# Kernel tuning notes

Hardware: AMD Instinct MI355X
Metric: run time of the kernel (lower is better)

Reference implementation:

```python
import jax, jax.numpy as jnp
from jax import lax
import numpy as np

B, L, C_IN, HID, RANK, NC = 256, 1024, 16, 512, 128, 10
PAD, K = 4, 7  # each conv block: L -> L + 2*PAD - K + 1 = L + 2


def _block(x, dwk, dwb, pwk, pwb, g, b):
    # x: (B, C, L); depthwise conv (groups=C) -> pointwise 1x1 -> batchnorm (batch stats) -> relu
    cin = dwk.shape[0]
    dn = ('NCH', 'OIH', 'NCH')
    y = lax.conv_general_dilated(x, dwk, (1,), [(PAD, PAD)], dimension_numbers=dn,
                                 feature_group_count=cin) + dwb[None, :, None]
    y = lax.conv_general_dilated(y, pwk, (1,), [(0, 0)], dimension_numbers=dn) + pwb[None, :, None]
    m = y.mean(axis=(0, 2), keepdims=True)
    v = y.var(axis=(0, 2), keepdims=True)
    y = (y - m) * lax.rsqrt(v + 1e-5) * g[None, :, None] + b[None, :, None]
    return jax.nn.relu(y)


def _cell(xp, h, c, Ui, Vi, Uh, Vh, bi, bh):
    # low-rank LSTM cell: W = U @ V kept factored for efficiency (same math)
    gates = (xp @ Ui) @ Vi + bi + (h @ Uh) @ Vh + bh  # (B, 4H)
    i, f, g, o = jnp.split(gates, 4, axis=1)
    c = jax.nn.sigmoid(f) * c + jax.nn.sigmoid(i) * jnp.tanh(g)
    h = jax.nn.sigmoid(o) * jnp.tanh(c)
    return h, c


def _forward(x, dw_k1, dw_b1, pw_k1, pw_b1, bn_g1, bn_b1,
             dw_k2, dw_b2, pw_k2, pw_b2, bn_g2, bn_b2,
             dw_k3, dw_b3, pw_k3, pw_b3, bn_g3, bn_b3,
             dw_k4, dw_b4, pw_k4, pw_b4, bn_g4, bn_b4,
             Ui1, Vi1, Uh1, Vh1, bi1, bh1,
             Ui2, Vi2, Uh2, Vh2, bi2, bh2,
             fc_w, fc_b):
    y = x[:, 0].transpose(0, 2, 1)  # (B, C_IN, L)
    y = _block(y, dw_k1, dw_b1, pw_k1, pw_b1, bn_g1, bn_b1)
    y = _block(y, dw_k2, dw_b2, pw_k2, pw_b2, bn_g2, bn_b2)
    y = _block(y, dw_k3, dw_b3, pw_k3, pw_b3, bn_g3, bn_b3)
    y = _block(y, dw_k4, dw_b4, pw_k4, pw_b4, bn_g4, bn_b4)
    # dropout = identity (eval)
    xs = y.transpose(2, 0, 1)  # (T, B, 32), T = L + 8
    bsz = xs.shape[1]
    z = jnp.zeros((bsz, HID), xs.dtype)

    def step(carry, xt):
        h1, c1, h2, c2 = carry
        h1, c1 = _cell(xt, h1, c1, Ui1, Vi1, Uh1, Vh1, bi1, bh1)
        h2, c2 = _cell(h1, h2, c2, Ui2, Vi2, Uh2, Vh2, bi2, bh2)
        return (h1, c1, h2, c2), None

    (h1, c1, h2, c2), _ = lax.scan(step, (z, z, z, z), xs)
    # original stacks all h2 then takes [:, -1, :] -> final h2; dropout = identity
    return h2 @ fc_w.T + fc_b  # (B, NC)


def setup_inputs() -> dict:
    key = jax.random.key(0)
    ks = iter(jax.random.split(key, 64))

    def n(shape, scale=0.05):
        return jax.random.normal(next(ks), shape, jnp.float32) * scale

    inp = {'x': jax.random.normal(next(ks), (B, 1, L, C_IN), jnp.float32)}
    chans = [C_IN, 32, 32, 32]
    for i, cin in enumerate(chans, start=1):
        inp[f'dw_k{i}'] = n((cin, 1, K))
        inp[f'dw_b{i}'] = jnp.zeros((cin,), jnp.float32)
        inp[f'pw_k{i}'] = n((32, cin, 1))
        inp[f'pw_b{i}'] = jnp.zeros((32,), jnp.float32)
        inp[f'bn_g{i}'] = jnp.ones((32,), jnp.float32)
        inp[f'bn_b{i}'] = jnp.zeros((32,), jnp.float32)
    inp['Ui1'] = n((32, RANK)); inp['Vi1'] = n((RANK, 4 * HID))
    inp['Uh1'] = n((HID, RANK)); inp['Vh1'] = n((RANK, 4 * HID))
    inp['bi1'] = jnp.zeros((4 * HID,), jnp.float32); inp['bh1'] = jnp.zeros((4 * HID,), jnp.float32)
    inp['Ui2'] = n((HID, RANK)); inp['Vi2'] = n((RANK, 4 * HID))
    inp['Uh2'] = n((HID, RANK)); inp['Vh2'] = n((RANK, 4 * HID))
    inp['bi2'] = jnp.zeros((4 * HID,), jnp.float32); inp['bh2'] = jnp.zeros((4 * HID,), jnp.float32)
    inp['fc_w'] = n((NC, HID)); inp['fc_b'] = jnp.zeros((NC,), jnp.float32)
    return inp


def reference(x, dw_k1, dw_b1, pw_k1, pw_b1, bn_g1, bn_b1,
              dw_k2, dw_b2, pw_k2, pw_b2, bn_g2, bn_b2,
              dw_k3, dw_b3, pw_k3, pw_b3, bn_g3, bn_b3,
              dw_k4, dw_b4, pw_k4, pw_b4, bn_g4, bn_b4,
              Ui1, Vi1, Uh1, Vh1, bi1, bh1,
              Ui2, Vi2, Uh2, Vh2, bi2, bh2,
              fc_w, fc_b):
    return _forward(x, dw_k1, dw_b1, pw_k1, pw_b1, bn_g1, bn_b1,
                    dw_k2, dw_b2, pw_k2, pw_b2, bn_g2, bn_b2,
                    dw_k3, dw_b3, pw_k3, pw_b3, bn_g3, bn_b3,
                    dw_k4, dw_b4, pw_k4, pw_b4, bn_g4, bn_b4,
                    Ui1, Vi1, Uh1, Vh1, bi1, bh1,
                    Ui2, Vi2, Uh2, Vh2, bi2, bh2,
                    fc_w, fc_b)
```

## Files before the change

### kernel.cpp

```cpp
#include <hip/hip_runtime.h>
#include <stdint.h>
#include <stddef.h>
#include <limits.h>

typedef _Float16 f16;
typedef _Float16 half8 __attribute__((ext_vector_type(8)));
typedef float floatx4 __attribute__((ext_vector_type(4)));
typedef unsigned long long u64;

#define MFMA(a,b,c) __builtin_amdgcn_mfma_f32_16x16x32_f16((a),(b),(c),0,0,0)

static constexpr int LMAX   = 1032;
static constexpr int TSTEPS = 1032;

static constexpr size_t ZBYTES   = (size_t)256*32*LMAX*2;
static constexpr size_t OFF_ZA   = 0;
static constexpr size_t OFF_ZB   = OFF_ZA + ZBYTES;
static constexpr size_t OFF_Y4   = OFF_ZA;
static constexpr size_t OFF_WH1F = OFF_ZB + ZBYTES;
static constexpr size_t OFF_WI2F = OFF_WH1F + (size_t)128*16*64*8*2;
static constexpr size_t OFF_WH2F = OFF_WI2F + (size_t)128*16*64*8*2;
static constexpr size_t OFF_WX1F = OFF_WH2F + (size_t)128*16*64*8*2;
static constexpr size_t OFF_B1   = OFF_WX1F + (size_t)128*64*8*2;
static constexpr size_t OFF_B2   = OFF_B1 + (size_t)2048*4;
static constexpr size_t OFF_STATS= OFF_B2 + (size_t)2048*4;
static constexpr size_t OFF_AB   = OFF_STATS + (size_t)4*64*4;
static constexpr size_t OFF_H1X  = OFF_AB + (size_t)4*64*4;
static constexpr size_t OFF_H2X  = OFF_H1X + (size_t)8*8*32*512*2;
static constexpr size_t OFF_FLAGS= OFF_H2X + (size_t)8*4*32*512*2;

__device__ __forceinline__ float sigm(float x){ return 1.f/(1.f+__expf(-x)); }
__device__ __forceinline__ float tanh_f(float x){ float e=__expf(2.f*x); return (e-1.f)/(e+1.f); }

__device__ __forceinline__ void sta64(void* p, u64 v){
  __hip_atomic_store((u64*)p, v, __ATOMIC_RELAXED, __HIP_MEMORY_SCOPE_AGENT);
}
__device__ __forceinline__ u64 lda64(const void* p){
  return __hip_atomic_load((const u64*)p, __ATOMIC_RELAXED, __HIP_MEMORY_SCOPE_AGENT);
}
__device__ __forceinline__ uint32_t ldf(const uint32_t* p){
  return __hip_atomic_load(p, __ATOMIC_RELAXED, __HIP_MEMORY_SCOPE_AGENT);
}
__device__ __forceinline__ void stf(uint32_t* p, uint32_t v){
  __hip_atomic_store(p, v, __ATOMIC_RELAXED, __HIP_MEMORY_SCOPE_AGENT);
}
__device__ __forceinline__ float4 ldg16(const void* p){
  float4 r;
  asm volatile("global_load_dwordx4 %0, %1, off sc0 sc1" : "=v"(r) : "v"(p) : "memory");
  return r;
}
__device__ __forceinline__ void vmcnt0(){
  asm volatile("s_waitcnt vmcnt(0)" ::: "memory");
}

__device__ __forceinline__ void pollWave(const uint32_t* fl, int t1, int t2){
  const int lane = threadIdx.x & 63;
  int tgt = (lane < 16) ? t1 : ((lane < 32) ? t2 : INT_MIN);
  if (tgt <= 0) tgt = INT_MIN;
  while (true){
    uint32_t v = ldf(&fl[lane & 31]);
    if (__all((int)v >= tgt)) break;
    __builtin_amdgcn_s_sleep(1);
  }
}

__device__ __forceinline__ void stageIssue(float4* r, const f16* src, int tid){
  #pragma unroll
  for (int i=0;i<8;++i){
    int qq = tid + 256*i;
    r[i] = ldg16(src + (size_t)qq*8);
  }
}
__device__ __forceinline__ void stageWrite(uint8_t* base, const float4* r, int tid){
  #pragma unroll
  for (int i=0;i<8;++i){
    int qq = tid + 256*i;
    int row = qq >> 6, ck = qq & 63;
    int cs = ck ^ (row & 15);
    *(float4*)(base + ((row<<6) + cs)*16) = r[i];
  }
}
__device__ __forceinline__ half8 fragLDS(const uint8_t* base, int row, int q, int lq){
  return *(const half8*)(base + (((row<<6)) + (((q<<2)+lq) ^ (row & 15)))*16);
}

__global__ void k_zero(float* stats, uint32_t* flags){
  int bx = blockIdx.x, tid = threadIdx.x;
  if (bx == 4){ if (tid < 256) stats[tid] = 0.f; }
  else flags[bx*256 + tid] = 0u;
}

__global__ __launch_bounds__(256) void k_prep_W(f16* __restrict__ dst, const float* __restrict__ U, const float* __restrict__ V){
  __shared__ float sU[64][65];
  __shared__ float sV[64][68];
  const int tid = threadIdx.x;
  const int n0 = blockIdx.x*64, k0 = blockIdx.y*64;
  const int tx = tid & 15, ty = tid >> 4;
  float acc[4][4];
  #pragma unroll
  for (int a=0;a<4;++a){ acc[a][0]=0.f; acc[a][1]=0.f; acc[a][2]=0.f; acc[a][3]=0.f; }
  for (int rc=0; rc<2; ++rc){
    __syncthreads();
    #pragma unroll
    for (int i=0;i<16;++i){
      int f = tid + 256*i;
      int row = f>>6, col = f&63;
      sU[row][col] = U[(size_t)(k0+row)*128 + rc*64 + col];
      sV[row][col] = V[(size_t)(rc*64+row)*2048 + n0 + col];
    }
    __syncthreads();
    for (int rr=0; rr<64; ++rr){
      float4 bv = *(const float4*)&sV[rr][tx*4];
      #pragma unroll
      for (int a=0;a<4;++a){
        float av = sU[ty*4+a][rr];
        acc[a][0] += av*bv.x; acc[a][1] += av*bv.y; acc[a][2] += av*bv.z; acc[a][3] += av*bv.w;
      }
    }
  }
  #pragma unroll
  for (int a=0;a<4;++a){
    int k = k0 + ty*4 + a;
    int q = k>>5, lq2 = (k>>3)&3, j = k&7;
    #pragma unroll
    for (int c=0;c<4;++c){
      int n = n0 + tx*4 + c;
      int nt = n>>4, lmn = n&15;
      dst[(((size_t)nt*16 + q)*64 + (lq2*16+lmn))*8 + j] = (f16)acc[a][c];
    }
  }
}

__global__ __launch_bounds__(256) void k_prep_Wx(f16* __restrict__ dst, const float* __restrict__ U, const float* __restrict__ V){
  __shared__ float sU[32][129];
  __shared__ float sV[128][68];
  const int tid = threadIdx.x, n0 = blockIdx.x*64;
  for (int f=tid; f<32*128; f+=256) sU[f>>7][f&127] = U[f];
  for (int f=tid; f<128*64; f+=256) sV[f>>6][f&63] = V[(size_t)(f>>6)*2048 + n0 + (f&63)];
  __syncthreads();
  int nn = tid & 63, kb = (tid>>6)*8;
  int n = n0 + nn;
  float acc[8];
  #pragma unroll
  for (int i=0;i<8;++i) acc[i]=0.f;
  for (int r=0;r<128;++r){
    float v = sV[r][nn];
    #pragma unroll
    for (int i=0;i<8;++i) acc[i] += sU[kb+i][r]*v;
  }
  int nt = n>>4, lmn = n&15;
  #pragma unroll
  for (int i=0;i<8;++i){
    int k = kb+i;
    dst[((size_t)nt*64 + (((k>>3)&3)*16 + lmn))*8 + (k&7)] = (f16)acc[i];
  }
}

__global__ void k_prep_bias(float* dst, const float* a, const float* b){
  int idx = blockIdx.x*256 + threadIdx.x;
  if (idx < 2048) dst[idx] = a[idx] + b[idx];
}

__global__ __launch_bounds__(256) void k_conv(
    const float* __restrict__ x0, const f16* __restrict__ zin,
    const float* __restrict__ abp,
    const float* __restrict__ dwk, const float* __restrict__ dwb,
    const float* __restrict__ pwk, const float* __restrict__ pwb,
    f16* __restrict__ zout, float* __restrict__ stats,
    int Lin, int Cin)
{
  const int tid = threadIdx.x;
  const int b = blockIdx.y;
  const int l = blockIdx.x*256 + tid;
  const int Lout = Lin + 2;
  __shared__ float sPw[32*32], sDw[32*7], sDb[32], sPb[32], sAb[64];
  __shared__ float sRed[2][4][32];
  for (int i=tid; i<Cin*32; i+=256) sPw[i] = pwk[i];
  for (int i=tid; i<Cin*7;  i+=256) sDw[i] = dwk[i];
  if (tid < Cin) sDb[tid] = dwb[tid];
  if (tid >= 64 && tid < 96) sPb[tid-64] = pwb[tid-64];
  if (abp != nullptr && tid >= 128 && tid < 192) sAb[tid-128] = abp[tid-128];
  __syncthreads();

  float acc[32];
  #pragma unroll
  for (int o=0;o<32;++o) acc[o] = sPb[o];
  const bool act = (l < Lout);
  if (act){
    for (int c=0;c<Cin;++c){
      float s = sDb[c];
      #pragma unroll
      for (int k=0;k<7;++k){
        int li = l + k - 4;
        float v = 0.f;
        if (li >= 0 && li < Lin){
          if (x0) v = x0[((size_t)b*1024 + li)*16 + c];
          else {
            float z = (float)zin[((size_t)b*32 + c)*LMAX + li];
            v = fmaxf(sAb[c]*z + sAb[32+c], 0.f);
          }
        }
        s += sDw[c*7+k]*v;
      }
      #pragma unroll
      for (int o=0;o<32;++o) acc[o] += sPw[o*Cin + c]*s;
    }
    #pragma unroll
    for (int o=0;o<32;++o) zout[((size_t)b*32 + o)*LMAX + l] = (f16)acc[o];
  }
  const int lane = tid & 63, wv = tid >> 6;
  for (int o=0;o<32;++o){
    float v = act ? acc[o] : 0.f;
    float q = v*v;
    #pragma unroll
    for (int m=1;m<64;m<<=1){ v += __shfl_xor(v,m); q += __shfl_xor(q,m); }
    if (lane == 0){ sRed[0][wv][o] = v; sRed[1][wv][o] = q; }
  }
  __syncthreads();
  if (tid < 32){
    float v = sRed[0][0][tid]+sRed[0][1][tid]+sRed[0][2][tid]+sRed[0][3][tid];
    float q = sRed[1][0][tid]+sRed[1][1][tid]+sRed[1][2][tid]+sRed[1][3][tid];
    atomicAdd(&stats[tid], v);
    atomicAdd(&stats[32+tid], q);
  }
}

__global__ void k_bnfin(const float* __restrict__ stats, const float* __restrict__ g,
                        const float* __restrict__ beta, float* __restrict__ ab, float inv_n)
{
  int o = threadIdx.x;
  if (o < 32){
    float m = stats[o]*inv_n;
    float var = stats[32+o]*inv_n - m*m;
    float a = g[o]*rsqrtf(var + 1e-5f);
    ab[o] = a; ab[32+o] = beta[o] - m*a;
  }
}

__global__ __launch_bounds__(256) void k_y4(const f16* __restrict__ z, const float* __restrict__ ab, f16* __restrict__ y){
  __shared__ f16 sT[32][264];
  __shared__ float sA[64];
  const int b = blockIdx.x, t0 = blockIdx.y*256, tid = threadIdx.x;
  if (tid < 64) sA[tid] = ab[tid];
  __syncthreads();
  #pragma unroll
  for (int i=0;i<8;++i){
    int f = tid + 256*i;
    int ch = f >> 6, tq = f & 63;
    int t = t0 + tq*4;
    if (t < 1032){
      u64 v = *(const u64*)(z + ((size_t)(b*32+ch)*1032 + t));
      union { u64 u; f16 h[4]; } cv; cv.u = v;
      float a = sA[ch], bb = sA[32+ch];
      #pragma unroll
      for (int j=0;j<4;++j) cv.h[j] = (f16)fmaxf(a*(float)cv.h[j] + bb, 0.f);
      *(u64*)&sT[ch][tq*4] = cv.u;
    }
  }
  __syncthreads();
  int t = t0 + tid;
  if (t < 1032){
    union { uint4 v; f16 h[8]; } o[4];
    #pragma unroll
    for (int k=0;k<4;++k)
      #pragma unroll
      for (int j=0;j<8;++j) o[k].h[j] = sT[k*8+j][t - t0];
    uint4* dst = (uint4*)(y + ((size_t)b*1032 + t)*32);
    #pragma unroll
    for (int k=0;k<4;++k) dst[k] = o[k].v;
  }
}

__global__ __launch_bounds__(256,1) void k_lstm(
  const f16* __restrict__ y4x,
  const f16* __restrict__ Wx1F, const f16* __restrict__ Wh1F,
  const f16* __restrict__ Wi2F, const f16* __restrict__ Wh2F,
  const float* __restrict__ bias1, const float* __restrict__ bias2,
  f16* __restrict__ h1x, f16* __restrict__ h2x,
  uint32_t* __restrict__ flags,
  const float* __restrict__ fcw, const float* __restrict__ fcb,
  float* __restrict__ outp)
{
  const int tid  = threadIdx.x;
  const int lane = tid & 63;
  const int w    = tid >> 6;
  const int lm   = lane & 15;
  const int lq   = lane >> 4;
  const int lq8  = lq*8;
  const int g    = blockIdx.x & 7;
  const int idx  = blockIdx.x >> 3;
  const int role = idx >> 4;
  const int b    = idx & 15;

  __shared__ __align__(16) uint8_t bufA[32768];
  __shared__ __align__(16) uint8_t bufB[32768];
  __shared__ float sGate[4*32*33];

  uint32_t* fl = flags + (size_t)g*32;

  const float* biasL = role ? bias2 : bias1;
  float bs[2];
  #pragma unroll
  for (int ct=0; ct<2; ++ct) bs[ct] = biasL[w*512 + b*32 + ct*16 + lm];

  const int nt0 = w*32 + b*2;
  f16* hdst_base = role ? h2x + (size_t)g*4*32*512 : h1x + (size_t)g*8*32*512;

  float creg[4] = {0.f,0.f,0.f,0.f};
  const int cr_row = tid >> 3, cr_u0 = (tid & 7)*4;

  if (role == 0){
    half8 wx[2];
    half8 wB[2][16];
    #pragma unroll
    for (int ct=0; ct<2; ++ct){
      wx[ct] = *(const half8*)&Wx1F[((size_t)(nt0+ct)*64 + lane)*8];
      #pragma unroll
      for (int q=0;q<16;++q)
        wB[ct][q] = *(const half8*)&Wh1F[(((size_t)(nt0+ct)*16 + q)*64 + lane)*8];
    }
    #pragma unroll 1
    for (int t=0; t<TSTEPS; ++t){
      half8 ya0 = *(const half8*)(y4x + ((size_t)(g*32 + lm)*1032 + t)*32 + lq8);
      half8 ya1 = *(const half8*)(y4x + ((size_t)(g*32 + 16 + lm)*1032 + t)*32 + lq8);
      if (w == 0) pollWave(fl, t, t-7);
      __syncthreads();
      float4 st[8];
      if (t >= 1) stageIssue(st, h1x + ((size_t)(g*8 + ((t-1)&7))*32*512), tid);
      floatx4 acc[2][2];
      #pragma unroll
      for (int ct=0; ct<2; ++ct){
        acc[ct][0] = (floatx4){bs[ct],bs[ct],bs[ct],bs[ct]};
        acc[ct][1] = acc[ct][0];
      }
      acc[0][0] = MFMA(ya0, wx[0], acc[0][0]);
      acc[0][1] = MFMA(ya1, wx[0], acc[0][1]);
      acc[1][0] = MFMA(ya0, wx[1], acc[1][0]);
      acc[1][1] = MFMA(ya1, wx[1], acc[1][1]);
      if (t >= 1){
        vmcnt0();
        stageWrite(bufA, st, tid);
      }
      __syncthreads();
      if (t >= 1){
        #pragma unroll
        for (int q=0;q<16;++q){
          half8 a0 = fragLDS(bufA, lm,    q, lq);
          half8 a1 = fragLDS(bufA, 16+lm, q, lq);
          acc[0][0] = MFMA(a0, wB[0][q], acc[0][0]);
          acc[0][1] = MFMA(a1, wB[0][q], acc[0][1]);
          acc[1][0] = MFMA(a0, wB[1][q], acc[1][0]);
          acc[1][1] = MFMA(a1, wB[1][q], acc[1][1]);
        }
      }
      __syncthreads();
      #pragma unroll
      for (int ct=0; ct<2; ++ct)
        #pragma unroll
        for (int rt=0; rt<2; ++rt)
          #pragma unroll
          for (int r=0;r<4;++r)
            sGate[w*1056 + (rt*16 + lq*4 + r)*33 + ct*16 + lm] = acc[ct][rt][r];
      __syncthreads();
      {
        union { u64 uu; f16 h[4]; } hv;
        #pragma unroll
        for (int j=0;j<4;++j){
          int u = cr_u0 + j;
          float iv = sGate[0*1056 + cr_row*33 + u];
          float fv = sGate[1*1056 + cr_row*33 + u];
          float gv = sGate[2*1056 + cr_row*33 + u];
          float ov = sGate[3*1056 + cr_row*33 + u];
          float c = sigm(fv)*creg[j] + sigm(iv)*tanh_f(gv);
          creg[j] = c;
          hv.h[j] = (f16)(sigm(ov)*tanh_f(c));
        }
        f16* dst = hdst_base + (size_t)(t&7)*32*512 + cr_row*512 + b*32 + cr_u0;
        sta64(dst, hv.uu);
      }
      vmcnt0();
      __syncthreads();
      if (tid == 0) stf(&fl[b], (uint32_t)(t+1));
    }
  } else {
    half8 wA[2][16];
    half8 wB[2][16];
    #pragma unroll
    for (int ct=0; ct<2; ++ct)
      #pragma unroll
      for (int q=0;q<16;++q){
        wA[ct][q] = *(const half8*)&Wi2F[(((size_t)(nt0+ct)*16 + q)*64 + lane)*8];
        wB[ct][q] = *(const half8*)&Wh2F[(((size_t)(nt0+ct)*16 + q)*64 + lane)*8];
      }
    #pragma unroll 1
    for (int t=0; t<TSTEPS; ++t){
      if (w == 0) pollWave(fl, t+1, t);
      __syncthreads();
      float4 s0[8], s1[8];
      stageIssue(s0, h1x + ((size_t)(g*8 + (t&7))*32*512), tid);
      if (t >= 1) stageIssue(s1, h2x + ((size_t)(g*4 + ((t-1)&3))*32*512), tid);
      vmcnt0();
      stageWrite(bufA, s0, tid);
      if (t >= 1) stageWrite(bufB, s1, tid);
      __syncthreads();
      floatx4 acc[2][2];
      #pragma unroll
      for (int ct=0; ct<2; ++ct){
        acc[ct][0] = (floatx4){bs[ct],bs[ct],bs[ct],bs[ct]};
        acc[ct][1] = acc[ct][0];
      }
      #pragma unroll
      for (int q=0;q<16;++q){
        half8 a0 = fragLDS(bufA, lm,    q, lq);
        half8 a1 = fragLDS(bufA, 16+lm, q, lq);
        acc[0][0] = MFMA(a0, wA[0][q], acc[0][0]);
        acc[0][1] = MFMA(a1, wA[0][q], acc[0][1]);
        acc[1][0] = MFMA(a0, wA[1][q], acc[1][0]);
        acc[1][1] = MFMA(a1, wA[1][q], acc[1][1]);
      }
      if (t >= 1){
        #pragma unroll
        for (int q=0;q<16;++q){
          half8 a0 = fragLDS(bufB, lm,    q, lq);
          half8 a1 = fragLDS(bufB, 16+lm, q, lq);
          acc[0][0] = MFMA(a0, wB[0][q], acc[0][0]);
          acc[0][1] = MFMA(a1, wB[0][q], acc[0][1]);
          acc[1][0] = MFMA(a0, wB[1][q], acc[1][0]);
          acc[1][1] = MFMA(a1, wB[1][q], acc[1][1]);
        }
      }
      __syncthreads();
      #pragma unroll
      for (int ct=0; ct<2; ++ct)
        #pragma unroll
        for (int rt=0; rt<2; ++rt)
          #pragma unroll
          for (int r=0;r<4;++r)
            sGate[w*1056 + (rt*16 + lq*4 + r)*33 + ct*16 + lm] = acc[ct][rt][r];
      __syncthreads();
      {
        union { u64 uu; f16 h[4]; } hv;
        #pragma unroll
        for (int j=0;j<4;++j){
          int u = cr_u0 + j;
          float iv = sGate[0*1056 + cr_row*33 + u];
          float fv = sGate[1*1056 + cr_row*33 + u];
          float gv = sGate[2*1056 + cr_row*33 + u];
          float ov = sGate[3*1056 + cr_row*33 + u];
          float c = sigm(fv)*creg[j] + sigm(iv)*tanh_f(gv);
          creg[j] = c;
          hv.h[j] = (f16)(sigm(ov)*tanh_f(c));
        }
        f16* dst = hdst_base + (size_t)(t&3)*32*512 + cr_row*512 + b*32 + cr_u0;
        sta64(dst, hv.uu);
      }
      vmcnt0();
      __syncthreads();
      if (tid == 0) stf(&fl[16 + b], (uint32_t)(t+1));
    }
    if (b == 0){
      if (w == 0) pollWave(fl, 0, TSTEPS);
      __syncthreads();
      const f16* hbase = h2x + ((size_t)(g*4 + ((TSTEPS-1)&3))*32*512);
      for (int e = tid; e < 320; e += 256){
        int row = e/10, nc = e%10;
        float s = fcb[nc];
        const float* wv = fcw + (size_t)nc*512;
        const u64* hp = (const u64*)(hbase + row*512);
        for (int k4=0;k4<128;++k4){
          union { u64 uu; f16 h[4]; } cv; cv.uu = lda64(hp + k4);
          #pragma unroll
          for (int i2=0;i2<4;++i2) s += (float)cv.h[i2]*wv[k4*4+i2];
        }
        outp[(size_t)(g*32+row)*10 + nc] = s;
      }
    }
  }
}

extern "C" void kernel_launch(void* const* d_in, const int* in_sizes, int n_in,
                              void* d_out, int out_size, void* d_ws, size_t ws_size,
                              hipStream_t stream)
{
  (void)in_sizes; (void)n_in; (void)out_size; (void)ws_size;
  const float* x = (const float*)d_in[0];
  auto F = [&](int i){ return (const float*)d_in[i]; };
  const float *Ui1=F(25), *Vi1=F(26), *Uh1=F(27), *Vh1=F(28), *bi1=F(29), *bh1=F(30);
  const float *Ui2=F(31), *Vi2=F(32), *Uh2=F(33), *Vh2=F(34), *bi2=F(35), *bh2=F(36);
  const float *fcw=F(37), *fcb=F(38);

  uint8_t* ws = (uint8_t*)d_ws;
  f16* zA   = (f16*)(ws + OFF_ZA);
  f16* zB   = (f16*)(ws + OFF_ZB);
  f16* y4x  = (f16*)(ws + OFF_Y4);
  f16* Wh1F = (f16*)(ws + OFF_WH1F);
  f16* Wi2F = (f16*)(ws + OFF_WI2F);
  f16* Wh2F = (f16*)(ws + OFF_WH2F);
  f16* Wx1F = (f16*)(ws + OFF_WX1F);
  float* bias1 = (float*)(ws + OFF_B1);
  float* bias2 = (float*)(ws + OFF_B2);
  float* stats = (float*)(ws + OFF_STATS);
  float* ab    = (float*)(ws + OFF_AB);
  f16* h1x  = (f16*)(ws + OFF_H1X);
  f16* h2x  = (f16*)(ws + OFF_H2X);
  uint32_t* flags = (uint32_t*)(ws + OFF_FLAGS);
  float* outp = (float*)d_out;

  k_zero<<<5, 256, 0, stream>>>(stats, flags);

  k_prep_W<<<dim3(32,8), 256, 0, stream>>>(Wh1F, Uh1, Vh1);
  k_prep_W<<<dim3(32,8), 256, 0, stream>>>(Wi2F, Ui2, Vi2);
  k_prep_W<<<dim3(32,8), 256, 0, stream>>>(Wh2F, Uh2, Vh2);
  k_prep_Wx<<<32, 256, 0, stream>>>(Wx1F, Ui1, Vi1);
  k_prep_bias<<<8, 256, 0, stream>>>(bias1, bi1, bh1);
  k_prep_bias<<<8, 256, 0, stream>>>(bias2, bi2, bh2);

  dim3 cgrid(5, 256);
  k_conv<<<cgrid, 256, 0, stream>>>(x, nullptr, nullptr, F(1), F(2), F(3), F(4),
                                    zA, stats + 0*64, 1024, 16);
  k_bnfin<<<1, 64, 0, stream>>>(stats + 0*64, F(5), F(6), ab + 0*64, 1.f/(256.f*1026.f));
  k_conv<<<cgrid, 256, 0, stream>>>(nullptr, zA, ab + 0*64, F(7), F(8), F(9), F(10),
                                    zB, stats + 1*64, 1026, 32);
  k_bnfin<<<1, 64, 0, stream>>>(stats + 1*64, F(11), F(12), ab + 1*64, 1.f/(256.f*1028.f));
  k_conv<<<cgrid, 256, 0, stream>>>(nullptr, zB, ab + 1*64, F(13), F(14), F(15), F(16),
                                    zA, stats + 2*64, 1028, 32);
  k_bnfin<<<1, 64, 0, stream>>>(stats + 2*64, F(17), F(18), ab + 2*64, 1.f/(256.f*1030.f));
  k_conv<<<cgrid, 256, 0, stream>>>(nullptr, zA, ab + 2*64, F(19), F(20), F(21), F(22),
                                    zB, stats + 3*64, 1030, 32);
  k_bnfin<<<1, 64, 0, stream>>>(stats + 3*64, F(23), F(24), ab + 3*64, 1.f/(256.f*1032.f));

  k_y4<<<dim3(256,5), 256, 0, stream>>>(zB, ab + 3*64, y4x);

  k_lstm<<<256, 256, 0, stream>>>(y4x,
                                  Wx1F, Wh1F, Wi2F, Wh2F,
                                  bias1, bias2,
                                  h1x, h2x, flags,
                                  fcw, fcb, outp);
}
```

Measured before the change: 6.149 ms.

## Keep LSTM weights low-rank and exchange rank projections via fixed-point atomic rings

The recurrent kernel no longer multiplies by dense 512x2048 weights rebuilt from U@V. Each block projects its hidden slice onto the rank-128 factor U and reduces partial projections across blocks with 64-bit fixed-point atomicAdd into zeroed ring buffers, then applies V locally. The batch split changes from 8 groups of 32 to 16 groups of 16 with 512-thread blocks, and gate math runs directly in MFMA registers instead of through shared memory. This cuts per-step matmul work and the volume of hidden state exchanged between blocks. In exchange it adds atomic traffic, ring zeroing, a fixed-point rounding error, and a deeper dependency chain per timestep.

Result: slower. 8.462 ms (+37.6%).

```diff
diff --git a/kernel.cpp b/kernel.cpp
--- a/kernel.cpp
+++ b/kernel.cpp
@@ -7,30 +7,45 @@
 typedef _Float16 half8 __attribute__((ext_vector_type(8)));
 typedef float floatx4 __attribute__((ext_vector_type(4)));
 typedef unsigned long long u64;
+typedef unsigned int u32;
 
 #define MFMA(a,b,c) __builtin_amdgcn_mfma_f32_16x16x32_f16((a),(b),(c),0,0,0)
 
 static constexpr int LMAX   = 1032;
 static constexpr int TSTEPS = 1032;
+
+static constexpr float FXSCALE = 1048576.0f;
+static constexpr float FXINV   = 1.0f/1048576.0f;
+static constexpr int   FXBIAS  = 1<<28;
+static constexpr int   FXBIAS4 = 1<<30;
 
 static constexpr size_t ZBYTES   = (size_t)256*32*LMAX*2;
 static constexpr size_t OFF_ZA   = 0;
 static constexpr size_t OFF_ZB   = OFF_ZA + ZBYTES;
 static constexpr size_t OFF_Y4   = OFF_ZA;
-static constexpr size_t OFF_WH1F = OFF_ZB + ZBYTES;
-static constexpr size_t OFF_WI2F = OFF_WH1F + (size_t)128*16*64*8*2;
-static constexpr size_t OFF_WH2F = OFF_WI2F + (size_t)128*16*64*8*2;
-static constexpr size_t OFF_WX1F = OFF_WH2F + (size_t)128*16*64*8*2;
-static constexpr size_t OFF_B1   = OFF_WX1F + (size_t)128*64*8*2;
-static constexpr size_t OFF_B2   = OFF_B1 + (size_t)2048*4;
-static constexpr size_t OFF_STATS= OFF_B2 + (size_t)2048*4;
-static constexpr size_t OFF_AB   = OFF_STATS + (size_t)4*64*4;
-static constexpr size_t OFF_H1X  = OFF_AB + (size_t)4*64*4;
-static constexpr size_t OFF_H2X  = OFF_H1X + (size_t)8*8*32*512*2;
-static constexpr size_t OFF_FLAGS= OFF_H2X + (size_t)8*4*32*512*2;
+static constexpr size_t OFF_WXF  = OFF_ZB + ZBYTES;
+static constexpr size_t OFF_VH1F = OFF_WXF  + 131072;
+static constexpr size_t OFF_VI2F = OFF_VH1F + 524288;
+static constexpr size_t OFF_VH2F = OFF_VI2F + 524288;
+static constexpr size_t OFF_UH1F = OFF_VH2F + 524288;
+static constexpr size_t OFF_UI2F = OFF_UH1F + 131072;
+static constexpr size_t OFF_UH2F = OFF_UI2F + 131072;
+static constexpr size_t OFF_B1   = OFF_UH2F + 131072;
+static constexpr size_t OFF_B2   = OFF_B1 + 8192;
+static constexpr size_t OFF_STATS= OFF_B2 + 8192;
+static constexpr size_t OFF_AB   = OFF_STATS + 1024;
+static constexpr size_t OFF_RINGS= OFF_AB + 1024;
+static constexpr size_t RING_BYTES = (size_t)16*24576*8;
+static constexpr size_t OFF_H2F  = OFF_RINGS + RING_BYTES;
+static constexpr size_t OFF_FLAGS= OFF_H2F + 262144;
 
 __device__ __forceinline__ float sigm(float x){ return 1.f/(1.f+__expf(-x)); }
-__device__ __forceinline__ float tanh_f(float x){ float e=__expf(2.f*x); return (e-1.f)/(e+1.f); }
+__device__ __forceinline__ float tanh_f(float x){
+  float ax = fabsf(x);
+  float e = __expf(-2.f*ax);
+  float r = (1.f - e)/(1.f + e);
+  return (x < 0.f) ? -r : r;
+}
 
 __device__ __forceinline__ void sta64(void* p, u64 v){
   __hip_atomic_store((u64*)p, v, __ATOMIC_RELAXED, __HIP_MEMORY_SCOPE_AGENT);
@@ -44,116 +59,96 @@
 __device__ __forceinline__ void stf(uint32_t* p, uint32_t v){
   __hip_atomic_store(p, v, __ATOMIC_RELAXED, __HIP_MEMORY_SCOPE_AGENT);
 }
-__device__ __forceinline__ float4 ldg16(const void* p){
-  float4 r;
+__device__ __forceinline__ int4 ldg16i(const void* p){
+  int4 r;
   asm volatile("global_load_dwordx4 %0, %1, off sc0 sc1" : "=v"(r) : "v"(p) : "memory");
   return r;
 }
 __device__ __forceinline__ void vmcnt0(){
   asm volatile("s_waitcnt vmcnt(0)" ::: "memory");
 }
-
-__device__ __forceinline__ void pollWave(const uint32_t* fl, int t1, int t2){
+__device__ __forceinline__ void schedbar(){
+  __builtin_amdgcn_sched_barrier(0);
+}
+
+__device__ __forceinline__ void pollWave8(const uint32_t* fl, int tP, int tC){
   const int lane = threadIdx.x & 63;
-  int tgt = (lane < 16) ? t1 : ((lane < 32) ? t2 : INT_MIN);
+  int tgt = (lane < 4) ? tP : ((lane < 8) ? tC : INT_MIN);
   if (tgt <= 0) tgt = INT_MIN;
   while (true){
-    uint32_t v = ldf(&fl[lane & 31]);
+    uint32_t v = ldf(&fl[lane & 7]);
     if (__all((int)v >= tgt)) break;
     __builtin_amdgcn_s_sleep(1);
   }
 }
 
-__device__ __forceinline__ void stageIssue(float4* r, const f16* src, int tid){
+__device__ __forceinline__ half8 pack8(int4 x, int4 y){
+  half8 h;
+  h[0] = (f16)((float)(x.x - FXBIAS4) * FXINV);
+  h[1] = (f16)((float)(x.y - FXBIAS4) * FXINV);
+  h[2] = (f16)((float)(x.z - FXBIAS4) * FXINV);
+  h[3] = (f16)((float)(x.w - FXBIAS4) * FXINV);
+  h[4] = (f16)((float)(y.x - FXBIAS4) * FXINV);
+  h[5] = (f16)((float)(y.y - FXBIAS4) * FXINV);
+  h[6] = (f16)((float)(y.z - FXBIAS4) * FXINV);
+  h[7] = (f16)((float)(y.w - FXBIAS4) * FXINV);
+  return h;
+}
+__device__ __forceinline__ u64 encodePair(float a, float b){
+  int ia = (int)rintf(a * FXSCALE) + FXBIAS;
+  int ib = (int)rintf(b * FXSCALE) + FXBIAS;
+  return (u64)(u32)ia | ((u64)(u32)ib << 32);
+}
+
+__device__ __forceinline__ int hT_byte(int row, int u){
+  return row*256 + ((((u>>3) ^ (row&7)))<<4) + (u&7)*2;
+}
+__device__ __forceinline__ half8 hT_frag(const uint8_t* hT, int lm, int q2, int lq){
+  return *(const half8*)(hT + lm*256 + ((((q2<<2)+lq) ^ (lm&7))<<4));
+}
+
+__global__ void k_zero(float* stats, uint32_t* flags, uint4* rings){
+  int bx = blockIdx.x, tid = threadIdx.x;
+  if (bx < 768){
+    rings[(size_t)bx*256 + tid] = (uint4){0u,0u,0u,0u};
+  } else {
+    if (tid < 256){ stats[tid] = 0.f; flags[tid] = 0u; flags[tid+256] = 0u; }
+  }
+}
+
+__global__ __launch_bounds__(256) void k_prep_wx(f16* __restrict__ dst, const float* __restrict__ U, const float* __restrict__ V){
+  int id = blockIdx.x*256 + threadIdx.x;
+  int n = id >> 2, lq = id & 3;
+  int nt = n >> 9, un = n & 511, b = un >> 7, w = (un >> 4) & 7, lm = un & 15;
+  float s[8];
   #pragma unroll
-  for (int i=0;i<8;++i){
-    int qq = tid + 256*i;
-    r[i] = ldg16(src + (size_t)qq*8);
-  }
-}
-__device__ __forceinline__ void stageWrite(uint8_t* base, const float4* r, int tid){
+  for (int j=0;j<8;++j) s[j]=0.f;
+  for (int r=0;r<128;++r){
+    float vv = V[(size_t)r*2048 + n];
+    #pragma unroll
+    for (int j=0;j<8;++j) s[j] += U[(size_t)(lq*8+j)*128 + r]*vv;
+  }
+  f16* o = dst + ((size_t)(((b*8+w)*4+nt)*64) + lq*16+lm)*8;
   #pragma unroll
-  for (int i=0;i<8;++i){
-    int qq = tid + 256*i;
-    int row = qq >> 6, ck = qq & 63;
-    int cs = ck ^ (row & 15);
-    *(float4*)(base + ((row<<6) + cs)*16) = r[i];
-  }
-}
-__device__ __forceinline__ half8 fragLDS(const uint8_t* base, int row, int q, int lq){
-  return *(const half8*)(base + (((row<<6)) + (((q<<2)+lq) ^ (row & 15)))*16);
-}
-
-__global__ void k_zero(float* stats, uint32_t* flags){
-  int bx = blockIdx.x, tid = threadIdx.x;
-  if (bx == 4){ if (tid < 256) stats[tid] = 0.f; }
-  else flags[bx*256 + tid] = 0u;
-}
-
-__global__ __launch_bounds__(256) void k_prep_W(f16* __restrict__ dst, const float* __restrict__ U, const float* __restrict__ V){
-  __shared__ float sU[64][65];
-  __shared__ float sV[64][68];
-  const int tid = threadIdx.x;
-  const int n0 = blockIdx.x*64, k0 = blockIdx.y*64;
-  const int tx = tid & 15, ty = tid >> 4;
-  float acc[4][4];
+  for (int j=0;j<8;++j) o[j] = (f16)s[j];
+}
+
+__global__ __launch_bounds__(256) void k_prep_v(f16* __restrict__ dst, const float* __restrict__ V){
+  int id = blockIdx.x*256 + threadIdx.x;
+  int n = id >> 4, kc = id & 15, q = kc >> 2, lq = kc & 3;
+  int nt = n >> 9, un = n & 511, b = un >> 7, w = (un >> 4) & 7, lm = un & 15;
+  f16* o = dst + ((size_t)((((b*8+w)*4+nt)*4+q)*64) + lq*16+lm)*8;
   #pragma unroll
-  for (int a=0;a<4;++a){ acc[a][0]=0.f; acc[a][1]=0.f; acc[a][2]=0.f; acc[a][3]=0.f; }
-  for (int rc=0; rc<2; ++rc){
-    __syncthreads();
-    #pragma unroll
-    for (int i=0;i<16;++i){
-      int f = tid + 256*i;
-      int row = f>>6, col = f&63;
-      sU[row][col] = U[(size_t)(k0+row)*128 + rc*64 + col];
-      sV[row][col] = V[(size_t)(rc*64+row)*2048 + n0 + col];
-    }
-    __syncthreads();
-    for (int rr=0; rr<64; ++rr){
-      float4 bv = *(const float4*)&sV[rr][tx*4];
-      #pragma unroll
-      for (int a=0;a<4;++a){
-        float av = sU[ty*4+a][rr];
-        acc[a][0] += av*bv.x; acc[a][1] += av*bv.y; acc[a][2] += av*bv.z; acc[a][3] += av*bv.w;
-      }
-    }
-  }
+  for (int j=0;j<8;++j) o[j] = (f16)V[(size_t)(q*32+lq*8+j)*2048 + n];
+}
+
+__global__ __launch_bounds__(256) void k_prep_u(f16* __restrict__ dst, const float* __restrict__ U){
+  int id = blockIdx.x*256 + threadIdx.x;
+  int rn = id >> 6, rest = id & 63, b = rest >> 4, q2 = (rest >> 2) & 3, lq = rest & 3;
+  int w = rn >> 4, lm = rn & 15;
+  f16* o = dst + ((size_t)(((b*8+w)*4+q2)*64) + lq*16+lm)*8;
   #pragma unroll
-  for (int a=0;a<4;++a){
-    int k = k0 + ty*4 + a;
-    int q = k>>5, lq2 = (k>>3)&3, j = k&7;
-    #pragma unroll
-    for (int c=0;c<4;++c){
-      int n = n0 + tx*4 + c;
-      int nt = n>>4, lmn = n&15;
-      dst[(((size_t)nt*16 + q)*64 + (lq2*16+lmn))*8 + j] = (f16)acc[a][c];
-    }
-  }
-}
-
-__global__ __launch_bounds__(256) void k_prep_Wx(f16* __restrict__ dst, const float* __restrict__ U, const float* __restrict__ V){
-  __shared__ float sU[32][129];
-  __shared__ float sV[128][68];
-  const int tid = threadIdx.x, n0 = blockIdx.x*64;
-  for (int f=tid; f<32*128; f+=256) sU[f>>7][f&127] = U[f];
-  for (int f=tid; f<128*64; f+=256) sV[f>>6][f&63] = V[(size_t)(f>>6)*2048 + n0 + (f&63)];
-  __syncthreads();
-  int nn = tid & 63, kb = (tid>>6)*8;
-  int n = n0 + nn;
-  float acc[8];
-  #pragma unroll
-  for (int i=0;i<8;++i) acc[i]=0.f;
-  for (int r=0;r<128;++r){
-    float v = sV[r][nn];
-    #pragma unroll
-    for (int i=0;i<8;++i) acc[i] += sU[kb+i][r]*v;
-  }
-  int nt = n>>4, lmn = n&15;
-  #pragma unroll
-  for (int i=0;i<8;++i){
-    int k = kb+i;
-    dst[((size_t)nt*64 + (((k>>3)&3)*16 + lmn))*8 + (k&7)] = (f16)acc[i];
-  }
+  for (int j=0;j<8;++j) o[j] = (f16)U[(size_t)(b*128 + q2*32 + lq*8 + j)*128 + rn];
 }
 
 __global__ void k_prep_bias(float* dst, const float* a, const float* b){
@@ -271,12 +266,13 @@
   }
 }
 
-__global__ __launch_bounds__(256,1) void k_lstm(
+__global__ __launch_bounds__(512,1) void k_lstm(
   const f16* __restrict__ y4x,
-  const f16* __restrict__ Wx1F, const f16* __restrict__ Wh1F,
-  const f16* __restrict__ Wi2F, const f16* __restrict__ Wh2F,
+  const f16* __restrict__ WxF,  const f16* __restrict__ VhF1,
+  const f16* __restrict__ ViF2, const f16* __restrict__ VhF2,
+  const f16* __restrict__ UhF1, const f16* __restrict__ UiF2, const f16* __restrict__ UhF2,
   const float* __restrict__ bias1, const float* __restrict__ bias2,
-  f16* __restrict__ h1x, f16* __restrict__ h2x,
+  u64* __restrict__ rings, f16* __restrict__ h2fin,
   uint32_t* __restrict__ flags,
   const float* __restrict__ fcw, const float* __restrict__ fcb,
   float* __restrict__ outp)
@@ -287,192 +283,222 @@
   const int lm   = lane & 15;
   const int lq   = lane >> 4;
   const int lq8  = lq*8;
-  const int g    = blockIdx.x & 7;
-  const int idx  = blockIdx.x >> 3;
-  const int role = idx >> 4;
-  const int b    = idx & 15;
-
-  __shared__ __align__(16) uint8_t bufA[32768];
-  __shared__ __align__(16) uint8_t bufB[32768];
-  __shared__ float sGate[4*32*33];
-
+  const int g    = blockIdx.x & 15;
+  const int idx  = blockIdx.x >> 4;
+  const int role = idx >> 2;
+  const int b    = idx & 3;
+
+  __shared__ __align__(16) uint8_t hT[4096];
+
+  u64* GB = rings + (size_t)g*24576;
   uint32_t* fl = flags + (size_t)g*32;
 
-  const float* biasL = role ? bias2 : bias1;
-  float bs[2];
-  #pragma unroll
-  for (int ct=0; ct<2; ++ct) bs[ct] = biasL[w*512 + b*32 + ct*16 + lm];
-
-  const int nt0 = w*32 + b*2;
-  f16* hdst_base = role ? h2x + (size_t)g*4*32*512 : h1x + (size_t)g*8*32*512;
-
-  float creg[4] = {0.f,0.f,0.f,0.f};
-  const int cr_row = tid >> 3, cr_u0 = (tid & 7)*4;
+  const int fb = (b*8 + w)*4;
 
   if (role == 0){
-    half8 wx[2];
-    half8 wB[2][16];
-    #pragma unroll
-    for (int ct=0; ct<2; ++ct){
-      wx[ct] = *(const half8*)&Wx1F[((size_t)(nt0+ct)*64 + lane)*8];
-      #pragma unroll
-      for (int q=0;q<16;++q)
-        wB[ct][q] = *(const half8*)&Wh1F[(((size_t)(nt0+ct)*16 + q)*64 + lane)*8];
-    }
+    half8 wx[4], wv[4][4], uh[4], ui[4];
+    float bs[4];
+    #pragma unroll
+    for (int nt=0; nt<4; ++nt){
+      wx[nt] = *(const half8*)&WxF[(((size_t)(fb+nt))*64 + lane)*8];
+      #pragma unroll
+      for (int q=0;q<4;++q)
+        wv[nt][q] = *(const half8*)&VhF1[((((size_t)(fb+nt))*4 + q)*64 + lane)*8];
+      bs[nt] = bias1[nt*512 + b*128 + w*16 + lm];
+    }
+    #pragma unroll
+    for (int q2=0;q2<4;++q2){
+      uh[q2] = *(const half8*)&UhF1[(((size_t)(fb+q2))*64 + lane)*8];
+      ui[q2] = *(const half8*)&UiF2[(((size_t)(fb+q2))*64 + lane)*8];
+    }
+    float creg[4] = {0.f,0.f,0.f,0.f};
+
     #pragma unroll 1
     for (int t=0; t<TSTEPS; ++t){
-      half8 ya0 = *(const half8*)(y4x + ((size_t)(g*32 + lm)*1032 + t)*32 + lq8);
-      half8 ya1 = *(const half8*)(y4x + ((size_t)(g*32 + 16 + lm)*1032 + t)*32 + lq8);
-      if (w == 0) pollWave(fl, t, t-7);
-      __syncthreads();
-      float4 st[8];
-      if (t >= 1) stageIssue(st, h1x + ((size_t)(g*8 + ((t-1)&7))*32*512), tid);
-      floatx4 acc[2][2];
-      #pragma unroll
-      for (int ct=0; ct<2; ++ct){
-        acc[ct][0] = (floatx4){bs[ct],bs[ct],bs[ct],bs[ct]};
-        acc[ct][1] = acc[ct][0];
-      }
-      acc[0][0] = MFMA(ya0, wx[0], acc[0][0]);
-      acc[0][1] = MFMA(ya1, wx[0], acc[0][1]);
-      acc[1][0] = MFMA(ya0, wx[1], acc[1][0]);
-      acc[1][1] = MFMA(ya1, wx[1], acc[1][1]);
+      half8 ya = *(const half8*)(y4x + ((size_t)(g*16+lm)*1032 + (size_t)t)*32 + lq8);
+      if (w == 0) pollWave8(fl, t, t-13);
+      __syncthreads();
+      {
+        int lin = b*512 + tid;
+        u64* zp = (lin < 1024) ? (GB + (size_t)((t+2)&3)*1024 + lin)
+                               : (GB + 4096 + (size_t)((t+2)&15)*1024 + (lin-1024));
+        sta64(zp, 0ull);
+      }
+      int4 rr[8];
+      if (t >= 1){
+        const char* rp = (const char*)(GB + (size_t)((t-1)&3)*1024) + lm*512;
+        #pragma unroll
+        for (int q=0;q<4;++q){
+          rr[2*q]   = ldg16i(rp + q*128 + lq*32);
+          rr[2*q+1] = ldg16i(rp + q*128 + lq*32 + 16);
+        }
+      }
+      floatx4 acc[4];
+      #pragma unroll
+      for (int nt=0;nt<4;++nt){
+        acc[nt] = (floatx4){bs[nt],bs[nt],bs[nt],bs[nt]};
+        acc[nt] = MFMA(ya, wx[nt], acc[nt]);
+      }
       if (t >= 1){
         vmcnt0();
-        stageWrite(bufA, st, tid);
-      }
-      __syncthreads();
-      if (t >= 1){
-        #pragma unroll
-        for (int q=0;q<16;++q){
-          half8 a0 = fragLDS(bufA, lm,    q, lq);
-          half8 a1 = fragLDS(bufA, 16+lm, q, lq);
-          acc[0][0] = MFMA(a0, wB[0][q], acc[0][0]);
-          acc[0][1] = MFMA(a1, wB[0][q], acc[0][1]);
-          acc[1][0] = MFMA(a0, wB[1][q], acc[1][0]);
-          acc[1][1] = MFMA(a1, wB[1][q], acc[1][1]);
-        }
-      }
-      __syncthreads();
-      #pragma unroll
-      for (int ct=0; ct<2; ++ct)
-        #pragma unroll
-        for (int rt=0; rt<2; ++rt)
+        schedbar();
+        #pragma unroll
+        for (int q=0;q<4;++q){
+          half8 aq = pack8(rr[2*q], rr[2*q+1]);
           #pragma unroll
-          for (int r=0;r<4;++r)
-            sGate[w*1056 + (rt*16 + lq*4 + r)*33 + ct*16 + lm] = acc[ct][rt][r];
-      __syncthreads();
-      {
-        union { u64 uu; f16 h[4]; } hv;
-        #pragma unroll
-        for (int j=0;j<4;++j){
-          int u = cr_u0 + j;
-          float iv = sGate[0*1056 + cr_row*33 + u];
-          float fv = sGate[1*1056 + cr_row*33 + u];
-          float gv = sGate[2*1056 + cr_row*33 + u];
-          float ov = sGate[3*1056 + cr_row*33 + u];
-          float c = sigm(fv)*creg[j] + sigm(iv)*tanh_f(gv);
-          creg[j] = c;
-          hv.h[j] = (f16)(sigm(ov)*tanh_f(c));
-        }
-        f16* dst = hdst_base + (size_t)(t&7)*32*512 + cr_row*512 + b*32 + cr_u0;
-        sta64(dst, hv.uu);
+          for (int nt=0;nt<4;++nt) acc[nt] = MFMA(aq, wv[nt][q], acc[nt]);
+        }
+      }
+      f16 hv[4];
+      #pragma unroll
+      for (int r=0;r<4;++r){
+        float iv = acc[0][r], fv = acc[1][r], gv = acc[2][r], ov = acc[3][r];
+        float c = sigm(fv)*creg[r] + sigm(iv)*tanh_f(gv);
+        creg[r] = c;
+        hv[r] = (f16)(sigm(ov)*tanh_f(c));
+      }
+      const int u = w*16 + lm;
+      #pragma unroll
+      for (int r=0;r<4;++r)
+        *(f16*)(hT + hT_byte(lq*4+r, u)) = hv[r];
+      __syncthreads();
+      floatx4 pH = {0.f,0.f,0.f,0.f}, pI = {0.f,0.f,0.f,0.f};
+      #pragma unroll
+      for (int q2=0;q2<4;++q2){
+        half8 ah = hT_frag(hT, lm, q2, lq);
+        pH = MFMA(ah, uh[q2], pH);
+        pI = MFMA(ah, ui[q2], pI);
+      }
+      float pHn[4], pIn[4];
+      #pragma unroll
+      for (int r=0;r<4;++r){ pHn[r] = __shfl_xor(pH[r],1); pIn[r] = __shfl_xor(pI[r],1); }
+      if (!(lane & 1)){
+        u64* s1 = GB + (size_t)(t&3)*1024;
+        u64* s2 = GB + 4096 + (size_t)(t&15)*1024;
+        const int ub = (w*16 + lm) >> 1;
+        #pragma unroll
+        for (int r=0;r<4;++r){
+          atomicAdd(s1 + (lq*4+r)*64 + ub, encodePair(pH[r], pHn[r]));
+          atomicAdd(s2 + (lq*4+r)*64 + ub, encodePair(pI[r], pIn[r]));
+        }
       }
       vmcnt0();
       __syncthreads();
       if (tid == 0) stf(&fl[b], (uint32_t)(t+1));
     }
   } else {
-    half8 wA[2][16];
-    half8 wB[2][16];
-    #pragma unroll
-    for (int ct=0; ct<2; ++ct)
-      #pragma unroll
-      for (int q=0;q<16;++q){
-        wA[ct][q] = *(const half8*)&Wi2F[(((size_t)(nt0+ct)*16 + q)*64 + lane)*8];
-        wB[ct][q] = *(const half8*)&Wh2F[(((size_t)(nt0+ct)*16 + q)*64 + lane)*8];
-      }
+    half8 wi[4][4], wv2[4][4], u2[4];
+    float bs[4];
+    #pragma unroll
+    for (int nt=0; nt<4; ++nt){
+      #pragma unroll
+      for (int q=0;q<4;++q){
+        wi[nt][q]  = *(const half8*)&ViF2[((((size_t)(fb+nt))*4 + q)*64 + lane)*8];
+        wv2[nt][q] = *(const half8*)&VhF2[((((size_t)(fb+nt))*4 + q)*64 + lane)*8];
+      }
+      bs[nt] = bias2[nt*512 + b*128 + w*16 + lm];
+    }
+    #pragma unroll
+    for (int q2=0;q2<4;++q2)
+      u2[q2] = *(const half8*)&UhF2[(((size_t)(fb+q2))*64 + lane)*8];
+    float creg[4] = {0.f,0.f,0.f,0.f};
+
     #pragma unroll 1
     for (int t=0; t<TSTEPS; ++t){
-      if (w == 0) pollWave(fl, t+1, t);
-      __syncthreads();
-      float4 s0[8], s1[8];
-      stageIssue(s0, h1x + ((size_t)(g*8 + (t&7))*32*512), tid);
-      if (t >= 1) stageIssue(s1, h2x + ((size_t)(g*4 + ((t-1)&3))*32*512), tid);
+      if (w == 0) pollWave8(fl, t+1, t);
+      __syncthreads();
+      { int lin = b*512 + tid;
+        if (lin < 1024) sta64(GB + 20480 + (size_t)((t+2)&3)*1024 + lin, 0ull); }
+      int4 ri[8], rh[8];
+      {
+        const char* rp = (const char*)(GB + 4096 + (size_t)(t&15)*1024) + lm*512;
+        #pragma unroll
+        for (int q=0;q<4;++q){
+          ri[2*q]   = ldg16i(rp + q*128 + lq*32);
+          ri[2*q+1] = ldg16i(rp + q*128 + lq*32 + 16);
+        }
+      }
+      if (t >= 1){
+        const char* rp = (const char*)(GB + 20480 + (size_t)((t-1)&3)*1024) + lm*512;
+        #pragma unroll
+        for (int q=0;q<4;++q){
+          rh[2*q]   = ldg16i(rp + q*128 + lq*32);
+          rh[2*q+1] = ldg16i(rp + q*128 + lq*32 + 16);
+        }
+      }
+      floatx4 acc[4];
+      #pragma unroll
+      for (int nt=0;nt<4;++nt) acc[nt] = (floatx4){bs[nt],bs[nt],bs[nt],bs[nt]};
+      if (t >= 1){ asm volatile("s_waitcnt vmcnt(8)" ::: "memory"); } else { vmcnt0(); }
+      schedbar();
+      #pragma unroll
+      for (int q=0;q<4;++q){
+        half8 aq = pack8(ri[2*q], ri[2*q+1]);
+        #pragma unroll
+        for (int nt=0;nt<4;++nt) acc[nt] = MFMA(aq, wi[nt][q], acc[nt]);
+      }
+      if (t >= 1){
+        vmcnt0();
+        schedbar();
+        #pragma unroll
+        for (int q=0;q<4;++q){
+          half8 aq = pack8(rh[2*q], rh[2*q+1]);
+          #pragma unroll
+          for (int nt=0;nt<4;++nt) acc[nt] = MFMA(aq, wv2[nt][q], acc[nt]);
+        }
+      }
+      f16 hv[4];
+      #pragma unroll
+      for (int r=0;r<4;++r){
+        float iv = acc[0][r], fv = acc[1][r], gv = acc[2][r], ov = acc[3][r];
+        float c = sigm(fv)*creg[r] + sigm(iv)*tanh_f(gv);
+        creg[r] = c;
+        hv[r] = (f16)(sigm(ov)*tanh_f(c));
+      }
+      const int u = w*16 + lm;
+      #pragma unroll
+      for (int r=0;r<4;++r)
+        *(f16*)(hT + hT_byte(lq*4+r, u)) = hv[r];
+      __syncthreads();
+      floatx4 p2 = {0.f,0.f,0.f,0.f};
+      #pragma unroll
+      for (int q2=0;q2<4;++q2){
+        half8 ah = hT_frag(hT, lm, q2, lq);
+        p2 = MFMA(ah, u2[q2], p2);
+      }
+      float p2n[4];
+      #pragma unroll
+      for (int r=0;r<4;++r) p2n[r] = __shfl_xor(p2[r],1);
+      if (!(lane & 1)){
+        u64* s3 = GB + 20480 + (size_t)(t&3)*1024;
+        const int ub = (w*16 + lm) >> 1;
+        #pragma unroll
+        for (int r=0;r<4;++r)
+          atomicAdd(s3 + (lq*4+r)*64 + ub, encodePair(p2[r], p2n[r]));
+      }
+      if (t == TSTEPS-1){
+        int row = tid >> 5, ug = (tid & 31)*4;
+        u64 v = *(const u64*)(hT + (row*256 + ((((ug>>3) ^ (row&7)))<<4) + (ug&7)*2));
+        sta64((u64*)(h2fin + ((size_t)(g*16+row)*512 + b*128 + ug)), v);
+      }
       vmcnt0();
-      stageWrite(bufA, s0, tid);
-      if (t >= 1) stageWrite(bufB, s1, tid);
-      __syncthreads();
-      floatx4 acc[2][2];
-      #pragma unroll
-      for (int ct=0; ct<2; ++ct){
-        acc[ct][0] = (floatx4){bs[ct],bs[ct],bs[ct],bs[ct]};
-        acc[ct][1] = acc[ct][0];
-      }
-      #pragma unroll
-      for (int q=0;q<16;++q){
-        half8 a0 = fragLDS(bufA, lm,    q, lq);
-        half8 a1 = fragLDS(bufA, 16+lm, q, lq);
-        acc[0][0] = MFMA(a0, wA[0][q], acc[0][0]);
-        acc[0][1] = MFMA(a1, wA[0][q], acc[0][1]);
-        acc[1][0] = MFMA(a0, wA[1][q], acc[1][0]);
-        acc[1][1] = MFMA(a1, wA[1][q], acc[1][1]);
-      }
-      if (t >= 1){
-        #pragma unroll
-        for (int q=0;q<16;++q){
-          half8 a0 = fragLDS(bufB, lm,    q, lq);
-          half8 a1 = fragLDS(bufB, 16+lm, q, lq);
-          acc[0][0] = MFMA(a0, wB[0][q], acc[0][0]);
-          acc[0][1] = MFMA(a1, wB[0][q], acc[0][1]);
-          acc[1][0] = MFMA(a0, wB[1][q], acc[1][0]);
-          acc[1][1] = MFMA(a1, wB[1][q], acc[1][1]);
-        }
-      }
-      __syncthreads();
-      #pragma unroll
-      for (int ct=0; ct<2; ++ct)
-        #pragma unroll
-        for (int rt=0; rt<2; ++rt)
-          #pragma unroll
-          for (int r=0;r<4;++r)
-            sGate[w*1056 + (rt*16 + lq*4 + r)*33 + ct*16 + lm] = acc[ct][rt][r];
-      __syncthreads();
-      {
-        union { u64 uu; f16 h[4]; } hv;
-        #pragma unroll
-        for (int j=0;j<4;++j){
-          int u = cr_u0 + j;
-          float iv = sGate[0*1056 + cr_row*33 + u];
-          float fv = sGate[1*1056 + cr_row*33 + u];
-          float gv = sGate[2*1056 + cr_row*33 + u];
-          float ov = sGate[3*1056 + cr_row*33 + u];
-          float c = sigm(fv)*creg[j] + sigm(iv)*tanh_f(gv);
-          creg[j] = c;
-          hv.h[j] = (f16)(sigm(ov)*tanh_f(c));
-        }
-        f16* dst = hdst_base + (size_t)(t&3)*32*512 + cr_row*512 + b*32 + cr_u0;
-        sta64(dst, hv.uu);
-      }
-      vmcnt0();
-      __syncthreads();
-      if (tid == 0) stf(&fl[16 + b], (uint32_t)(t+1));
+      __syncthreads();
+      if (tid == 0) stf(&fl[4+b], (uint32_t)(t+1));
     }
     if (b == 0){
-      if (w == 0) pollWave(fl, 0, TSTEPS);
-      __syncthreads();
-      const f16* hbase = h2x + ((size_t)(g*4 + ((TSTEPS-1)&3))*32*512);
-      for (int e = tid; e < 320; e += 256){
+      if (w == 0) pollWave8(fl, 0, TSTEPS);
+      __syncthreads();
+      for (int e = tid; e < 160; e += 512){
         int row = e/10, nc = e%10;
         float s = fcb[nc];
-        const float* wv = fcw + (size_t)nc*512;
-        const u64* hp = (const u64*)(hbase + row*512);
+        const float* wvv = fcw + (size_t)nc*512;
+        const u64* hp = (const u64*)(h2fin + (size_t)(g*16+row)*512);
         for (int k4=0;k4<128;++k4){
           union { u64 uu; f16 h[4]; } cv; cv.uu = lda64(hp + k4);
           #pragma unroll
-          for (int i2=0;i2<4;++i2) s += (float)cv.h[i2]*wv[k4*4+i2];
-        }
-        outp[(size_t)(g*32+row)*10 + nc] = s;
+          for (int i2=0;i2<4;++i2) s += (float)cv.h[i2]*wvv[k4*4+i2];
+        }
+        outp[(size_t)(g*16+row)*10 + nc] = s;
       }
     }
   }
@@ -493,25 +519,31 @@
   f16* zA   = (f16*)(ws + OFF_ZA);
   f16* zB   = (f16*)(ws + OFF_ZB);
   f16* y4x  = (f16*)(ws + OFF_Y4);
-  f16* Wh1F = (f16*)(ws + OFF_WH1F);
-  f16* Wi2F = (f16*)(ws + OFF_WI2F);
-  f16* Wh2F = (f16*)(ws + OFF_WH2F);
-  f16* Wx1F = (f16*)(ws + OFF_WX1F);
+  f16* WxF  = (f16*)(ws + OFF_WXF);
+  f16* Vh1F = (f16*)(ws + OFF_VH1F);
+  f16* Vi2F = (f16*)(ws + OFF_VI2F);
+  f16* Vh2F = (f16*)(ws + OFF_VH2F);
+  f16* Uh1F = (f16*)(ws + OFF_UH1F);
+  f16* Ui2F = (f16*)(ws + OFF_UI2F);
+  f16* Uh2F = (f16*)(ws + OFF_UH2F);
   float* bias1 = (float*)(ws + OFF_B1);
   float* bias2 = (float*)(ws + OFF_B2);
   float* stats = (float*)(ws + OFF_STATS);
   float* ab    = (float*)(ws + OFF_AB);
-  f16* h1x  = (f16*)(ws + OFF_H1X);
-  f16* h2x  = (f16*)(ws + OFF_H2X);
+  u64* rings   = (u64*)(ws + OFF_RINGS);
+  f16* h2fin   = (f16*)(ws + OFF_H2F);
   uint32_t* flags = (uint32_t*)(ws + OFF_FLAGS);
   float* outp = (float*)d_out;
 
-  k_zero<<<5, 256, 0, stream>>>(stats, flags);
-
-  k_prep_W<<<dim3(32,8), 256, 0, stream>>>(Wh1F, Uh1, Vh1);
-  k_prep_W<<<dim3(32,8), 256, 0, stream>>>(Wi2F, Ui2, Vi2);
-  k_prep_W<<<dim3(32,8), 256, 0, stream>>>(Wh2F, Uh2, Vh2);
-  k_prep_Wx<<<32, 256, 0, stream>>>(Wx1F, Ui1, Vi1);
+  k_zero<<<769, 256, 0, stream>>>(stats, flags, (uint4*)rings);
+
+  k_prep_wx<<<32, 256, 0, stream>>>(WxF, Ui1, Vi1);
+  k_prep_v<<<128, 256, 0, stream>>>(Vh1F, Vh1);
+  k_prep_v<<<128, 256, 0, stream>>>(Vi2F, Vi2);
+  k_prep_v<<<128, 256, 0, stream>>>(Vh2F, Vh2);
+  k_prep_u<<<32, 256, 0, stream>>>(Uh1F, Uh1);
+  k_prep_u<<<32, 256, 0, stream>>>(Ui2F, Ui2);
+  k_prep_u<<<32, 256, 0, stream>>>(Uh2F, Uh2);
   k_prep_bias<<<8, 256, 0, stream>>>(bias1, bi1, bh1);
   k_prep_bias<<<8, 256, 0, stream>>>(bias2, bi2, bh2);
 
@@ -531,9 +563,10 @@
 
   k_y4<<<dim3(256,5), 256, 0, stream>>>(zB, ab + 3*64, y4x);
 
-  k_lstm<<<256, 256, 0, stream>>>(y4x,
-                                  Wx1F, Wh1F, Wi2F, Wh2F,
+  k_lstm<<<128, 512, 0, stream>>>(y4x,
+                                  WxF, Vh1F, Vi2F, Vh2F,
+                                  Uh1F, Ui2F, Uh2F,
                                   bias1, bias2,
-                                  h1x, h2x, flags,
+                                  rings, h2fin, flags,
                                   fcw, fcb, outp);
 }
```
